# Performance work log

Hardware: AMD Instinct MI355X
Metric: run time of the kernel (lower is better)

Reference implementation:

```python
import jax, jax.numpy as jnp
import numpy as np

N_HEADS = 32
N_KV = 8
HEAD_DIM = 128
ROPE_THETA = 10000.0
PAST_LEN = 2048


def _rope_cos_sin(position_ids):
    # inv_freq: [head_dim/2]
    inv_freq = 1.0 / (ROPE_THETA ** (jnp.arange(0, HEAD_DIM, 2, dtype=jnp.float32) / HEAD_DIM))
    freqs = position_ids.astype(jnp.float32)[..., None] * inv_freq  # [B, S, hd/2]
    emb = jnp.concatenate([freqs, freqs], axis=-1)  # [B, S, hd]
    return jnp.cos(emb), jnp.sin(emb)


def _rotate_half(x):
    x1, x2 = jnp.split(x, 2, axis=-1)
    return jnp.concatenate([-x2, x1], axis=-1)


def setup_inputs() -> dict:
    key = jax.random.key(0)
    ks = jax.random.split(key, 10)
    B, S = 1, 2048
    IN = 8192
    s = 0.02
    return {
        "hidden_states": jax.random.normal(ks[0], (B, S, IN), jnp.float32),
        "position_ids": (jnp.arange(S, dtype=jnp.int32) + PAST_LEN)[None, :],
        "cache_k": jax.random.normal(ks[1], (B, N_KV, PAST_LEN, HEAD_DIM), jnp.float32),
        "cache_v": jax.random.normal(ks[2], (B, N_KV, PAST_LEN, HEAD_DIM), jnp.float32),
        "Wq": jax.random.normal(ks[3], (N_HEADS * HEAD_DIM, IN), jnp.float32) * s,
        "bq": jax.random.normal(ks[4], (N_HEADS * HEAD_DIM,), jnp.float32) * s,
        "Wk": jax.random.normal(ks[5], (N_KV * HEAD_DIM, IN), jnp.float32) * s,
        "bk": jax.random.normal(ks[6], (N_KV * HEAD_DIM,), jnp.float32) * s,
        "Wv": jax.random.normal(ks[7], (N_KV * HEAD_DIM, IN), jnp.float32) * s,
        "bv": jax.random.normal(ks[8], (N_KV * HEAD_DIM,), jnp.float32) * s,
        "Wo": jax.random.normal(ks[9], (N_HEADS * HEAD_DIM, N_HEADS * HEAD_DIM), jnp.float32) * s,
    }


def reference(hidden_states, position_ids, cache_k, cache_v, Wq, bq, Wk, bk, Wv, bv, Wo):
    B, Sq, _ = hidden_states.shape
    G = N_HEADS // N_KV

    # QKV projections -> [B, H, S, D]
    q = (hidden_states @ Wq.T + bq).reshape(B, Sq, N_HEADS, HEAD_DIM).transpose(0, 2, 1, 3)
    k = (hidden_states @ Wk.T + bk).reshape(B, Sq, N_KV, HEAD_DIM).transpose(0, 2, 1, 3)
    v = (hidden_states @ Wv.T + bv).reshape(B, Sq, N_KV, HEAD_DIM).transpose(0, 2, 1, 3)

    # RoPE
    cos, sin = _rope_cos_sin(position_ids)  # [B, Sq, D]
    cos, sin = cos[:, None], sin[:, None]   # broadcast over heads
    q = q * cos + _rotate_half(q) * sin
    k = k * cos + _rotate_half(k) * sin

    # KV cache concat
    key = jnp.concatenate([cache_k, k], axis=2)   # [B, Kv, Sk, D]
    value = jnp.concatenate([cache_v, v], axis=2)
    Sk = key.shape[2]
    past_len = Sk - Sq

    # GQA attention (grouped einsum == repeat_interleave + SDPA)
    qg = q.reshape(B, N_KV, G, Sq, HEAD_DIM)
    scale = 1.0 / jnp.sqrt(jnp.float32(HEAD_DIM))
    scores = jnp.einsum("bkgqd,bkld->bkgql", qg, key) * scale  # [B, Kv, G, Sq, Sk]

    q_pos = past_len + jnp.arange(Sq)
    mask = jnp.arange(Sk)[None, :] <= q_pos[:, None]  # [Sq, Sk]
    scores = jnp.where(mask[None, None, None], scores, -jnp.inf)
    attn = jax.nn.softmax(scores, axis=-1)

    ctx = jnp.einsum("bkgql,bkld->bkgqd", attn, value)
    ctx = ctx.reshape(B, N_HEADS, Sq, HEAD_DIM).transpose(0, 2, 1, 3).reshape(B, Sq, N_HEADS * HEAD_DIM)
    out = ctx @ Wo.T
    return out, key, value
```

## Files before the change

kernel.cpp:

```cpp
#include <hip/hip_runtime.h>
#include <hip/hip_bf16.h>
#include <math.h>

typedef float f32x4 __attribute__((ext_vector_type(4)));
typedef short s16x8 __attribute__((ext_vector_type(8)));
typedef unsigned short u16x8 __attribute__((ext_vector_type(8)));
typedef __bf16 bf16x8 __attribute__((ext_vector_type(8)));

__device__ __forceinline__ unsigned short f2bf(float f) {
  return __builtin_bit_cast(unsigned short, (__bf16)f);
}

__device__ __forceinline__ f32x4 mfma16(s16x8 a, s16x8 b, f32x4 c) {
  return __builtin_amdgcn_mfma_f32_16x16x32_bf16(
      __builtin_bit_cast(bf16x8, a), __builtin_bit_cast(bf16x8, b), c, 0, 0, 0);
}

#define GLDS(gp, lp) __builtin_amdgcn_global_load_lds(                      \
    (__attribute__((address_space(1))) void*)(gp),                          \
    (__attribute__((address_space(3))) void*)(lp), 16, 0, 0)

struct __attribute__((aligned(8))) us4 { unsigned short x, y, z, w; };
__device__ __forceinline__ us4 cvt4(float4 v) {
  us4 r; r.x = f2bf(v.x); r.y = f2bf(v.y); r.z = f2bf(v.z); r.w = f2bf(v.w);
  return r;
}
__device__ __forceinline__ u16x8 cvt8(float4 a, float4 b) {
  u16x8 r;
  r[0] = f2bf(a.x); r[1] = f2bf(a.y); r[2] = f2bf(a.z); r[3] = f2bf(a.w);
  r[4] = f2bf(b.x); r[5] = f2bf(b.y); r[6] = f2bf(b.z); r[7] = f2bf(b.w);
  return r;
}

__global__ __launch_bounds__(256) void conv_all(
    const float4* __restrict__ h, const float4* __restrict__ bq,
    const float4* __restrict__ bk, const float4* __restrict__ bv,
    us4* __restrict__ hbf, float4* __restrict__ biasc)
{
  const unsigned int U = 4195840u;
  const unsigned int stride = gridDim.x * blockDim.x;
  for (unsigned int u = blockIdx.x * blockDim.x + threadIdx.x; u < U; u += stride) {
    if (u < 4194304u) {
      hbf[u] = cvt4(h[u]);
    } else {
      unsigned int o = u - 4194304u;
      float4 v = (o < 1024u) ? bq[o] : (o < 1280u) ? bk[o - 1024u] : bv[o - 1280u];
      biasc[o] = v;
    }
  }
}

__global__ __launch_bounds__(256) void rope_table(const int* __restrict__ pos_ids,
                                                  float* __restrict__ cost,
                                                  float* __restrict__ sint)
{
  int idx = blockIdx.x * blockDim.x + threadIdx.x;
  if (idx >= 131072) return;
  int s = idx >> 6, i = idx & 63;
  double invf = exp(-((double)i / 64.0) * 9.210340371976184);
  double ang = (double)pos_ids[s] * invf;
  cost[idx] = (float)cos(ang);
  sint[idx] = (float)sin(ang);
}

template<int NF>
__global__ __launch_bounds__(512, 2) void gemm_wf(const unsigned short* __restrict__ A,
                                                  const float* __restrict__ B0,
                                                  const float* __restrict__ B1,
                                                  const float* __restrict__ B2,
                                                  int r1, int r2,
                                                  const float* __restrict__ bias,
                                                  float* __restrict__ C,
                                                  int M, int N, int K)
{
  constexpr int BN = NF * 64;
  constexpr int BUFSZ = 32768 + BN * 128;
  __shared__ char smem[2 * BUFSZ];
  const int tid = threadIdx.x;
  const int l = tid & 63;
  const int w = tid >> 6;
  const int wm = w >> 2, wn = w & 3;
  const int wr = wm * 128;
  const int wc = wn * (16 * NF);
  const int lk16 = (l >> 4) * 16;

  const int nwg = gridDim.x;
  const int s = (blockIdx.x & 7) * (nwg >> 3) + (blockIdx.x >> 3);
  const int NBY = M >> 8;
  const int by = s % NBY, bx = s / NBY;
  const size_t arow0 = (size_t)by * 256;
  const int brow0 = bx * BN;
  const size_t Kb = (size_t)K * 2;
  const char* Ab = (const char*)A;

  const float* bptr[NF];
#pragma unroll
  for (int cc = 0; cc < NF; ++cc) {
    const int ch = cc * 512 + tid;
    const int r = ch >> 3;
    const int rg = brow0 + r;
    const float* bp; int rl;
    if (rg < r1)      { bp = B0; rl = rg; }
    else if (rg < r2) { bp = B1; rl = rg - r1; }
    else              { bp = B2; rl = rg - r2; }
    bptr[cc] = bp + (size_t)rl * K + (ch & 7) * 8;
  }

  f32x4 acc[8][NF];
#pragma unroll
  for (int i = 0; i < 8; ++i)
#pragma unroll
    for (int j = 0; j < NF; ++j) acc[i][j] = (f32x4){0.f, 0.f, 0.f, 0.f};

  float4 breg[NF][2];

  auto STAGE_A = [&](int t, char* buf) {
    const size_t k0b = (size_t)t * 128;
#pragma unroll
    for (int cc = 0; cc < 4; ++cc) {
      const int ch = cc * 512 + tid;
      const int r = ch >> 3;
      const int c2s = ((ch & 7) * 16) ^ ((r & 7) << 4);
      GLDS(Ab + (arow0 + r) * Kb + k0b + c2s, buf + ch * 16);
    }
  };
  auto B_LOAD = [&](int t) {
#pragma unroll
    for (int cc = 0; cc < NF; ++cc) {
      const float* p = bptr[cc] + t * 64;
      breg[cc][0] = *(const float4*)p;
      breg[cc][1] = *(const float4*)(p + 4);
    }
  };
  auto B_WRITE = [&](char* buf) {
#pragma unroll
    for (int cc = 0; cc < NF; ++cc) {
      const int ch = cc * 512 + tid;
      const int r = ch >> 3;
      const int off = ((ch & 7) * 16) ^ ((r & 7) << 4);
      *(u16x8*)(buf + 32768 + r * 128 + off) = cvt8(breg[cc][0], breg[cc][1]);
    }
  };

  const int nt = K >> 6;
  B_LOAD(0);
  STAGE_A(0, smem);
  asm volatile("s_waitcnt vmcnt(0)" ::: "memory");
  B_WRITE(smem);
  asm volatile("s_waitcnt lgkmcnt(0)" ::: "memory");
  __builtin_amdgcn_s_barrier();

  for (int t = 0; t < nt; ++t) {
    char* cur = smem + (t & 1) * BUFSZ;
    char* nxt = smem + ((t + 1) & 1) * BUFSZ;
    if (t + 1 < nt) { B_LOAD(t + 1); STAGE_A(t + 1, nxt); }
    s16x8 bfr[NF][2];
#pragma unroll
    for (int n = 0; n < NF; ++n)
#pragma unroll
      for (int k = 0; k < 2; ++k) {
        const int r = wc + n * 16 + (l & 15);
        const int c2 = k * 64 + lk16;
        bfr[n][k] = *(const s16x8*)(cur + 32768 + (r * 128 + (c2 ^ ((r & 7) << 4))));
      }
#pragma unroll
    for (int qd = 0; qd < 4; ++qd) {
      s16x8 afr[2][2];
#pragma unroll
      for (int i = 0; i < 2; ++i)
#pragma unroll
        for (int k = 0; k < 2; ++k) {
          const int r = wr + (qd * 2 + i) * 16 + (l & 15);
          const int c2 = k * 64 + lk16;
          afr[i][k] = *(const s16x8*)(cur + (r * 128 + (c2 ^ ((r & 7) << 4))));
        }
      __builtin_amdgcn_s_setprio(1);
#pragma unroll
      for (int i = 0; i < 2; ++i)
#pragma unroll
        for (int n = 0; n < NF; ++n)
#pragma unroll
          for (int k = 0; k < 2; ++k)
            acc[qd * 2 + i][n] = mfma16(afr[i][k], bfr[n][k], acc[qd * 2 + i][n]);
      __builtin_amdgcn_s_setprio(0);
      if (qd == 1 && t + 1 < nt) {
        B_WRITE(nxt);
      }
    }
    asm volatile("s_waitcnt vmcnt(0) lgkmcnt(0)" ::: "memory");
    __builtin_amdgcn_s_barrier();
  }

  const int r0 = (int)arow0 + wr + (l >> 4) * 4;
  const int c0 = brow0 + wc + (l & 15);
#pragma unroll
  for (int mi = 0; mi < 8; ++mi) {
#pragma unroll
    for (int ni = 0; ni < NF; ++ni) {
      const int c = c0 + ni * 16;
      const float bvv = bias ? bias[c] : 0.f;
#pragma unroll
      for (int rr = 0; rr < 4; ++rr) {
        const int r = r0 + mi * 16 + rr;
        C[(size_t)r * N + c] = acc[mi][ni][rr] + bvv;
      }
    }
  }
}

__global__ __launch_bounds__(256) void rope_scatter(
    const float* __restrict__ qkv, const float* __restrict__ cost,
    const float* __restrict__ sint, const float* __restrict__ cache_k,
    const float* __restrict__ cache_v, float* __restrict__ keyout,
    float* __restrict__ valout, unsigned short* __restrict__ qbf,
    char* __restrict__ kswz, char* __restrict__ vswz)
{
  const float rs = 0.08838834764831845f;
  const int stride = gridDim.x * blockDim.x;
  for (int idx = blockIdx.x * blockDim.x + threadIdx.x; idx < 11534336; idx += stride) {
    if (idx < 4194304) {
      int i = idx & 63, hh = (idx >> 6) & 31, s = idx >> 11;
      const float* base = qkv + (size_t)s * 6144 + hh * 128 + i;
      float q1 = base[0], q2 = base[64];
      float c = cost[s * 64 + i], sn = sint[s * 64 + i];
      float o1 = (q1 * c - q2 * sn) * rs, o2 = (q2 * c + q1 * sn) * rs;
      unsigned short* qd = qbf + ((size_t)hh * 2048 + s) * 128 + i;
      qd[0] = f2bf(o1); qd[64] = f2bf(o2);
    } else if (idx < 5242880) {
      int j = idx - 4194304;
      int i = j & 63, kh = (j >> 6) & 7, s = j >> 9;
      const float* base = qkv + (size_t)s * 6144 + 4096 + kh * 128 + i;
      float k1 = base[0], k2 = base[64];
      float c = cost[s * 64 + i], sn = sint[s * 64 + i];
      float o1 = k1 * c - k2 * sn, o2 = k2 * c + k1 * sn;
      float* kd = keyout + ((size_t)kh * 4096 + 2048 + s) * 128 + i;
      kd[0] = o1; kd[64] = o2;
      int t = 32 + (s >> 6), r = s & 63;
      char* tb = kswz + (size_t)(kh * 64 + t) * 16384;
      *(unsigned short*)(tb + ((r * 256 + i * 2) ^ ((r & 7) << 4))) = f2bf(o1);
      *(unsigned short*)(tb + ((r * 256 + (i + 64) * 2) ^ ((r & 7) << 4))) = f2bf(o2);
    } else if (idx < 7340032) {
      int j = idx - 5242880;
      int d = j & 127, kh = (j >> 7) & 7, s = j >> 10;
      float v = qkv[(size_t)s * 6144 + 5120 + kh * 128 + d];
      valout[((size_t)kh * 4096 + 2048 + s) * 128 + d] = v;
      int t = 32 + (s >> 6), c = s & 63;
      char* tb = vswz + (size_t)(kh * 64 + t) * 16384;
      *(unsigned short*)(tb + ((d * 128 + c * 2) ^ ((d & 7) << 4))) = f2bf(v);
    } else if (idx < 9437184) {
      int j = idx - 7340032;
      int d = j & 127, s = (j >> 7) & 2047, kh = j >> 18;
      float v = cache_k[(size_t)(kh * 2048 + s) * 128 + d];
      keyout[((size_t)kh * 4096 + s) * 128 + d] = v;
      int t = s >> 6, r = s & 63;
      char* tb = kswz + (size_t)(kh * 64 + t) * 16384;
      *(unsigned short*)(tb + ((r * 256 + d * 2) ^ ((r & 7) << 4))) = f2bf(v);
    } else {
      int j = idx - 9437184;
      int d = j & 127, s = (j >> 7) & 2047, kh = j >> 18;
      float v = cache_v[(size_t)(kh * 2048 + s) * 128 + d];
      valout[((size_t)kh * 4096 + s) * 128 + d] = v;
      int t = s >> 6, c = s & 63;
      char* tb = vswz + (size_t)(kh * 64 + t) * 16384;
      *(unsigned short*)(tb + ((d * 128 + c * 2) ^ ((d & 7) << 4))) = f2bf(v);
    }
  }
}

__global__ __launch_bounds__(512) void attn_fwd(const unsigned short* __restrict__ qbf,
                                                const char* __restrict__ kswz,
                                                const char* __restrict__ vswz,
                                                unsigned short* __restrict__ ctx)
{
  __shared__ char smem[81920];
  char* Ps = smem + 65536;
  const int tid = threadIdx.x;
  const int l = tid & 63;
  const int w = tid >> 6;
  const int d = blockIdx.x;
  const int b = d >> 5;
  const int qt = (b < 8) ? b : 23 - b;
  const int h = (d & 7) * 4 + ((d >> 3) & 3);
  const int kh = h >> 2;
  const int nt = 2 * qt + 34;
  const int qrow16 = (l >> 4) * 4;
  const float L2E = 1.44269504f;
  const float M16 = 23.0831098f;

  s16x8 aq[4];
  {
    const int qr = qt * 128 + w * 16 + (l & 15);
    const unsigned short* qp = qbf + ((size_t)h * 2048 + qr) * 128 + (l >> 4) * 8;
#pragma unroll
    for (int kc = 0; kc < 4; ++kc) aq[kc] = *(const s16x8*)(qp + kc * 32);
  }
  f32x4 o[8];
#pragma unroll
  for (int i = 0; i < 8; ++i) o[i] = (f32x4){0.f, 0.f, 0.f, 0.f};
  float ls[4] = {0.f, 0.f, 0.f, 0.f};

  const char* kb0 = kswz + (size_t)kh * (64 * 16384);
  const char* vb0 = vswz + (size_t)kh * (64 * 16384);
  char* Pw = Ps + w * 2048;

  auto STAGE = [&](int t, int c) {
    const char* kb = kb0 + (size_t)t * 16384;
    const char* vb = vb0 + (size_t)t * 16384;
    char* Kt = smem + c * 32768;
    char* Vt = Kt + 16384;
#pragma unroll
    for (int j = 0; j < 2; ++j) {
      const int cw = j * 8 + w;
      GLDS(kb + (cw * 64 + l) * 16, Kt + cw * 1024);
      GLDS(vb + (cw * 64 + l) * 16, Vt + cw * 1024);
    }
  };

  STAGE(0, 0);
  int c = 0;
  for (int t = 0; t < nt; ++t) {
    asm volatile("s_waitcnt vmcnt(0)" ::: "memory");
    __builtin_amdgcn_s_barrier();
    asm volatile("" ::: "memory");
    if (t + 1 < nt) STAGE(t + 1, c ^ 1);
    const char* Kt = smem + c * 32768;
    const char* Vt = Kt + 16384;

    f32x4 s[4];
#pragma unroll
    for (int i = 0; i < 4; ++i) s[i] = (f32x4){0.f, 0.f, 0.f, 0.f};
    __builtin_amdgcn_s_setprio(1);
#pragma unroll
    for (int kc = 0; kc < 4; ++kc) {
      const int d0b = (kc * 32 + (l >> 4) * 8) * 2;
#pragma unroll
      for (int ni = 0; ni < 4; ++ni) {
        const int row = ni * 16 + (l & 15);
        s16x8 kf = *(const s16x8*)(Kt + ((row * 256 + d0b) ^ ((row & 7) << 4)));
        s[ni] = mfma16(aq[kc], kf, s[ni]);
      }
    }
    __builtin_amdgcn_s_setprio(0);
    if (t >= nt - 2) {
      const int qpos_b = 2048 + qt * 128 + w * 16 + qrow16;
      const int kvcol = (l & 15);
#pragma unroll
      for (int ni = 0; ni < 4; ++ni) {
        const int kvpos = t * 64 + ni * 16 + kvcol;
#pragma unroll
        for (int rr = 0; rr < 4; ++rr)
          if (kvpos > qpos_b + rr) s[ni][rr] = -1e30f;
      }
    }
#pragma unroll
    for (int ni = 0; ni < 4; ++ni) {
      const int colb = (ni * 16 + (l & 15)) * 2;
#pragma unroll
      for (int rr = 0; rr < 4; ++rr) {
        const float p = __builtin_amdgcn_exp2f(__builtin_fmaf(s[ni][rr], L2E, -M16));
        ls[rr] += p;
        const int q = qrow16 + rr;
        *(__bf16*)(Pw + ((q * 128 + colb) ^ ((q & 7) << 4))) = (__bf16)p;
      }
    }
    s16x8 pa[2];
#pragma unroll
    for (int kc2 = 0; kc2 < 2; ++kc2) {
      const int q = l & 15;
      const int kvb = (kc2 * 32 + (l >> 4) * 8) * 2;
      pa[kc2] = *(const s16x8*)(Pw + ((q * 128 + kvb) ^ ((q & 7) << 4)));
    }
    __builtin_amdgcn_s_setprio(1);
#pragma unroll
    for (int sub = 0; sub < 8; ++sub) {
      const int dd = sub * 16 + (l & 15);
#pragma unroll
      for (int kc2 = 0; kc2 < 2; ++kc2) {
        const int kvb = (kc2 * 32 + (l >> 4) * 8) * 2;
        s16x8 vf = *(const s16x8*)(Vt + ((dd * 128 + kvb) ^ ((dd & 7) << 4)));
        o[sub] = mfma16(pa[kc2], vf, o[sub]);
      }
    }
    __builtin_amdgcn_s_setprio(0);
    asm volatile("" ::: "memory");
    c ^= 1;
  }

#pragma unroll
  for (int rr = 0; rr < 4; ++rr) {
    float v = ls[rr];
    v += __shfl_xor(v, 1);
    v += __shfl_xor(v, 2);
    v += __shfl_xor(v, 4);
    v += __shfl_xor(v, 8);
    ls[rr] = 1.0f / v;
  }
  const int r0 = qt * 128 + w * 16 + qrow16;
  const int c0 = h * 128 + (l & 15);
#pragma unroll
  for (int sub = 0; sub < 8; ++sub)
#pragma unroll
    for (int rr = 0; rr < 4; ++rr) {
      const float v = o[sub][rr] * ls[rr];
      ctx[(size_t)(r0 + rr) * 4096 + c0 + sub * 16] = f2bf(v);
    }
}

extern "C" void kernel_launch(void* const* d_in, const int* in_sizes, int n_in,
                              void* d_out, int out_size, void* d_ws, size_t ws_size,
                              hipStream_t stream) {
  (void)in_sizes; (void)n_in; (void)out_size; (void)ws_size;
  const float* hs     = (const float*)d_in[0];
  const int*   pos    = (const int*)d_in[1];
  const float* cachek = (const float*)d_in[2];
  const float* cachev = (const float*)d_in[3];
  const float* Wq     = (const float*)d_in[4];
  const float* bq     = (const float*)d_in[5];
  const float* Wk     = (const float*)d_in[6];
  const float* bk     = (const float*)d_in[7];
  const float* Wv     = (const float*)d_in[8];
  const float* bv     = (const float*)d_in[9];
  const float* Wo     = (const float*)d_in[10];

  float* out    = (float*)d_out;
  float* keyout = out + (size_t)2048 * 4096;
  float* valout = keyout + (size_t)8 * 4096 * 128;

  char* ws = (char*)d_ws;
  unsigned short* hbf    = (unsigned short*)(ws + 0);
  unsigned short* qbf    = (unsigned short*)(ws + 0);
  char*           kswz   = ws + 16777216;
  char*           vswz   = ws + 25165824;
  float*          qkvf   = (float*)(ws + 167772160);
  unsigned short* ctxbf  = (unsigned short*)(ws + 167772160);
  float*          cost   = (float*)(ws + 218103808);
  float*          sint   = (float*)(ws + 218628096);
  float*          biasc  = (float*)(ws + 219152384);

  conv_all<<<2048, 256, 0, stream>>>((const float4*)hs, (const float4*)bq,
                                     (const float4*)bk, (const float4*)bv,
                                     (us4*)hbf, (float4*)biasc);
  rope_table<<<512, 256, 0, stream>>>(pos, cost, sint);
  gemm_wf<3><<<256, 512, 0, stream>>>(hbf, Wq, Wk, Wv, 4096, 5120, biasc, qkvf,
                                      2048, 6144, 8192);
  rope_scatter<<<2048, 256, 0, stream>>>(qkvf, cost, sint, cachek, cachev,
                                         keyout, valout, qbf, kswz, vswz);
  attn_fwd<<<512, 512, 0, stream>>>(qbf, kswz, vswz, ctxbf);
  gemm_wf<2><<<256, 512, 0, stream>>>(ctxbf, Wo, Wo, Wo, 1 << 30, 1 << 30, nullptr,
                                      out, 2048, 4096, 4096);
}
```

Baseline: 585.2 us.

## Prefetch GEMM B tiles two steps ahead with ping-pong registers

The fp32 B-operand register prefetch in the QKV/output GEMM now runs two K-tiles ahead, using two alternating register buffers. The main loop is unrolled by two so each tile writes the previously loaded buffer to LDS while loading the other. The bf16 conversion and LDS write of B move from mid-compute to the start of each tile. The minimum-occupancy hint of two blocks per CU is dropped so the compiler can spend more registers on the extra buffer. The loop still ends each tile with a full vmcnt(0) wait, so the deeper prefetch may not add overlap. The extra registers may also lower occupancy.

```diff
diff --git a/kernel.cpp b/kernel.cpp
--- a/kernel.cpp
+++ b/kernel.cpp
@@ -64,14 +64,14 @@
 }
 
 template<int NF>
-__global__ __launch_bounds__(512, 2) void gemm_wf(const unsigned short* __restrict__ A,
-                                                  const float* __restrict__ B0,
-                                                  const float* __restrict__ B1,
-                                                  const float* __restrict__ B2,
-                                                  int r1, int r2,
-                                                  const float* __restrict__ bias,
-                                                  float* __restrict__ C,
-                                                  int M, int N, int K)
+__global__ __launch_bounds__(512) void gemm_wf(const unsigned short* __restrict__ A,
+                                               const float* __restrict__ B0,
+                                               const float* __restrict__ B1,
+                                               const float* __restrict__ B2,
+                                               int r1, int r2,
+                                               const float* __restrict__ bias,
+                                               float* __restrict__ C,
+                                               int M, int N, int K)
 {
   constexpr int BN = NF * 64;
   constexpr int BUFSZ = 32768 + BN * 128;
@@ -112,7 +112,7 @@
 #pragma unroll
     for (int j = 0; j < NF; ++j) acc[i][j] = (f32x4){0.f, 0.f, 0.f, 0.f};
 
-  float4 breg[NF][2];
+  float4 bregA[NF][2], bregB[NF][2];
 
   auto STAGE_A = [&](int t, char* buf) {
     const size_t k0b = (size_t)t * 128;
@@ -124,36 +124,42 @@
       GLDS(Ab + (arow0 + r) * Kb + k0b + c2s, buf + ch * 16);
     }
   };
-  auto B_LOAD = [&](int t) {
+  auto B_LOAD = [&](int t, float4 (&br)[NF][2]) {
 #pragma unroll
     for (int cc = 0; cc < NF; ++cc) {
       const float* p = bptr[cc] + t * 64;
-      breg[cc][0] = *(const float4*)p;
-      breg[cc][1] = *(const float4*)(p + 4);
+      br[cc][0] = *(const float4*)p;
+      br[cc][1] = *(const float4*)(p + 4);
     }
   };
-  auto B_WRITE = [&](char* buf) {
+  auto B_WRITE = [&](char* buf, float4 (&br)[NF][2]) {
 #pragma unroll
     for (int cc = 0; cc < NF; ++cc) {
       const int ch = cc * 512 + tid;
       const int r = ch >> 3;
       const int off = ((ch & 7) * 16) ^ ((r & 7) << 4);
-      *(u16x8*)(buf + 32768 + r * 128 + off) = cvt8(breg[cc][0], breg[cc][1]);
+      *(u16x8*)(buf + 32768 + r * 128 + off) = cvt8(br[cc][0], br[cc][1]);
     }
   };
 
   const int nt = K >> 6;
-  B_LOAD(0);
+
+  B_LOAD(0, bregA);
   STAGE_A(0, smem);
   asm volatile("s_waitcnt vmcnt(0)" ::: "memory");
-  B_WRITE(smem);
+  B_WRITE(smem, bregA);
   asm volatile("s_waitcnt lgkmcnt(0)" ::: "memory");
   __builtin_amdgcn_s_barrier();
-
-  for (int t = 0; t < nt; ++t) {
+  B_LOAD(1, bregA);
+
+  auto TILE = [&](int t, float4 (&brW)[NF][2], float4 (&brL)[NF][2]) {
     char* cur = smem + (t & 1) * BUFSZ;
     char* nxt = smem + ((t + 1) & 1) * BUFSZ;
-    if (t + 1 < nt) { B_LOAD(t + 1); STAGE_A(t + 1, nxt); }
+    if (t + 2 < nt) B_LOAD(t + 2, brL);
+    if (t + 1 < nt) {
+      STAGE_A(t + 1, nxt);
+      B_WRITE(nxt, brW);
+    }
     s16x8 bfr[NF][2];
 #pragma unroll
     for (int n = 0; n < NF; ++n)
@@ -183,12 +189,14 @@
           for (int k = 0; k < 2; ++k)
             acc[qd * 2 + i][n] = mfma16(afr[i][k], bfr[n][k], acc[qd * 2 + i][n]);
       __builtin_amdgcn_s_setprio(0);
-      if (qd == 1 && t + 1 < nt) {
-        B_WRITE(nxt);
-      }
     }
     asm volatile("s_waitcnt vmcnt(0) lgkmcnt(0)" ::: "memory");
     __builtin_amdgcn_s_barrier();
+  };
+
+  for (int t = 0; t < nt; t += 2) {
+    TILE(t, bregA, bregB);
+    TILE(t + 1, bregB, bregA);
   }
 
   const int r0 = (int)arow0 + wr + (l >> 4) * 4;
```

After: 631.2 us. +7.8%, slower.
